# Optimization experiments

Hardware: AMD Instinct MI355X
Metric: run time of the kernel (lower is better)

## Reference

```python
import jax, jax.numpy as jnp
import numpy as np

B, S, D, H = 2, 1024, 1024, 16
HD = D // H
WINDOW = 256
FFN = 4 * D


def setup_inputs() -> dict:
    key = jax.random.key(0)
    ks = jax.random.split(key, 12)
    xav = lambda k, o, i: jax.random.normal(k, (o, i), jnp.float32) * np.sqrt(2.0 / (o + i))
    return {
        "x": jax.random.normal(ks[0], (B, S, D), jnp.float32),
        "wq": xav(ks[1], D, D), "bq": jnp.zeros((D,), jnp.float32),
        "wk": xav(ks[2], D, D), "bk": jnp.zeros((D,), jnp.float32),
        "wv": xav(ks[3], D, D), "bv": jnp.zeros((D,), jnp.float32),
        "wo": xav(ks[4], D, D), "bo": jnp.zeros((D,), jnp.float32),
        "attn_norm_w": jnp.ones((D,), jnp.float32),
        "ffn_norm_w": jnp.ones((D,), jnp.float32),
        "gate_w": xav(ks[5], FFN, D),
        "up_w": xav(ks[6], FFN, D),
        "down_w": xav(ks[7], D, FFN),
    }


def _rms(x, w):
    return x * jax.lax.rsqrt(jnp.mean(x * x, axis=-1, keepdims=True) + 1e-6) * w


def _rotate_half(x):
    x1, x2 = jnp.split(x, 2, axis=-1)
    return jnp.concatenate([-x2, x1], axis=-1)


def _rope_cos_sin(seq_len, head_dim):
    inv_freq = 1.0 / (10000.0 ** (jnp.arange(0, head_dim, 2, dtype=jnp.float32) / head_dim))
    freqs = jnp.arange(seq_len, dtype=jnp.float32)[:, None] * inv_freq[None, :]  # [S, HD/2]
    emb = jnp.concatenate([freqs, freqs], axis=-1)  # [S, HD]
    return jnp.cos(emb)[None, None], jnp.sin(emb)[None, None]  # [1,1,S,HD]


def reference(x, wq, bq, wk, bk, wv, bv, wo, bo, attn_norm_w, ffn_norm_w, gate_w, up_w, down_w):
    b, s, d = x.shape
    scale = 1.0 / np.sqrt(HD)
    residual = x
    h = _rms(x, attn_norm_w)
    q = (h @ wq.T + bq).reshape(b, s, H, HD).transpose(0, 2, 1, 3)  # [B,H,S,HD]
    k = (h @ wk.T + bk).reshape(b, s, H, HD).transpose(0, 2, 1, 3)
    v = (h @ wv.T + bv).reshape(b, s, H, HD).transpose(0, 2, 1, 3)
    cos, sin = _rope_cos_sin(s, HD)
    q = q * cos + _rotate_half(q) * sin
    k = k * cos + _rotate_half(k) * sin
    scores = jnp.einsum("bhqd,bhkd->bhqk", q, k) * scale  # dense [B,H,S,S]
    i = jnp.arange(s)[:, None]
    j = jnp.arange(s)[None, :]
    local_mask = (j <= i) & (i - j < WINDOW)  # causal sliding window
    scores = jnp.where(local_mask[None, None], scores, -jnp.inf)
    attn = jax.nn.softmax(scores, axis=-1)
    out = jnp.einsum("bhqk,bhkd->bhqd", attn, v)
    out = out.transpose(0, 2, 1, 3).reshape(b, s, d) @ wo.T + bo
    x = residual + out
    residual = x
    h = _rms(x, ffn_norm_w)
    ffn = (jax.nn.silu(h @ gate_w.T) * (h @ up_w.T)) @ down_w.T
    return (residual + ffn, attn)
```

## Files before the change

kernel.cpp:

```cpp
#include <hip/hip_runtime.h>

typedef unsigned short u16;
typedef unsigned int u32;
typedef __attribute__((ext_vector_type(8))) short short8;
typedef __attribute__((ext_vector_type(4))) float f32x4;

__device__ __forceinline__ float b2fu(u32 u) {
  union { u32 i; float f; } v; v.i = u << 16; return v.f;
}
__device__ __forceinline__ u16 f2bu(float f) {
  union { float f; u32 i; } v; v.f = f;
  u32 r = (v.i + 0x7fffu + ((v.i >> 16) & 1u)) >> 16;
  return (u16)r;
}
__device__ __forceinline__ void gl_lds16(const void* g, void* l) {
  __builtin_amdgcn_global_load_lds((const __attribute__((address_space(1))) void*)g,
                                   (__attribute__((address_space(3))) void*)l, 16, 0, 0);
}
__device__ __forceinline__ short8 ld_lds_b8(const u16* p) {
  uint2 a = *(const uint2*)p;
  uint2 b = *(const uint2*)(p + 4);
  union { u32 u[4]; short8 s; } v;
  v.u[0] = a.x; v.u[1] = a.y; v.u[2] = b.x; v.u[3] = b.y;
  return v.s;
}

__global__ __launch_bounds__(256) void cvt_weights(
    const float* __restrict__ wq, const float* __restrict__ wk,
    const float* __restrict__ wv, const float* __restrict__ wo,
    const float* __restrict__ wg, const float* __restrict__ wu,
    const float* __restrict__ wd, u16* __restrict__ dst,
    const float* __restrict__ bq, const float* __restrict__ bk,
    const float* __restrict__ bv, float* __restrict__ bqkv)
{
  if (blockIdx.x >= 16384) {
    const int s = blockIdx.x - 16384;
    const float* bsrc = (s == 0) ? bq : (s == 1) ? bk : bv;
    const int o = threadIdx.x * 4;
    *(float4*)(bqkv + s * 1024 + o) = *(const float4*)(bsrc + o);
    return;
  }
  size_t e = ((size_t)blockIdx.x * 256 + threadIdx.x) * 4;
  size_t seg = e >> 20;
  const float* src; size_t soff;
  if      (seg == 0) { src = wq; soff = e; }
  else if (seg == 1) { src = wk; soff = e - ((size_t)1 << 20); }
  else if (seg == 2) { src = wv; soff = e - ((size_t)2 << 20); }
  else if (seg == 3) { src = wo; soff = e - ((size_t)3 << 20); }
  else if (seg < 12) {
    size_t idx = e - ((size_t)4 << 20);
    int rc = (int)(idx >> 10);
    int col = (int)(idx & 1023);
    int bi = rc >> 5, j = rc & 31;
    if (j < 16) { src = wg; soff = (size_t)(bi * 16 + j) * 1024 + col; }
    else        { src = wu; soff = (size_t)(bi * 16 + j - 16) * 1024 + col; }
  }
  else { src = wd; soff = e - ((size_t)12 << 20); }
  float4 v = *(const float4*)(src + soff);
  *(ushort4*)(dst + e) = make_ushort4(f2bu(v.x), f2bu(v.y), f2bu(v.z), f2bu(v.w));
}

__global__ __launch_bounds__(256) void rmsnorm_kernel(
    const float* __restrict__ x, const float* __restrict__ w, u16* __restrict__ out)
{
  const int row = blockIdx.x;
  const int t = threadIdx.x;
  float4 v = ((const float4*)(x + (size_t)row * 1024))[t];
  float ss = v.x * v.x + v.y * v.y + v.z * v.z + v.w * v.w;
#pragma unroll
  for (int m = 32; m > 0; m >>= 1) ss += __shfl_xor(ss, m, 64);
  __shared__ float red[4];
  if ((t & 63) == 0) red[t >> 6] = ss;
  __syncthreads();
  float tot = red[0] + red[1] + red[2] + red[3];
  float r = rsqrtf(tot * (1.0f / 1024.0f) + 1e-6f);
  float4 wv = ((const float4*)w)[t];
  ushort4 o = make_ushort4(f2bu(v.x * r * wv.x), f2bu(v.y * r * wv.y),
                           f2bu(v.z * r * wv.z), f2bu(v.w * r * wv.w));
  ((ushort4*)(out + (size_t)row * 1024))[t] = o;
}

template<int TMB, int TNB, int EPI, bool HAS_BIAS, bool HAS_RES, bool SPLIT>
__global__ __launch_bounds__(256) void gemm_bt(
    const u16* __restrict__ A, const u16* __restrict__ B, float* __restrict__ C,
    const float* __restrict__ bias, const float* __restrict__ res,
    int M, int N, int K, int lda,
    u16* __restrict__ P0, u16* __restrict__ P1, u16* __restrict__ P2)
{
  constexpr int BK = 32;
  constexpr int WTM = TMB / 2, WTN = TNB / 2;
  constexpr int MT = WTM / 16, NT = WTN / 16;
  __shared__ u16 As[TMB * BK];
  __shared__ u16 Bs[TNB * BK];
  const int t = threadIdx.x;
  const int w = t >> 6, l = t & 63;
  const int wm = (w >> 1) * WTM, wn = (w & 1) * WTN;
  const int lr = l & 15, lq = l >> 4;
  const int tile_m = blockIdx.y * TMB, tile_n = blockIdx.x * TNB;
  const int kb = SPLIT ? blockIdx.z * K : 0;
  if (SPLIT) C += (size_t)blockIdx.z * M * N;

  f32x4 acc[MT][NT] = {};

  const int sr = t >> 2;
  const int scs = (((t & 3) ^ ((t >> 3) & 3)) * 8);
  const int rsw = (lq ^ ((lr >> 1) & 3)) * 8;
  const u16* Ab = A + (size_t)(tile_m + sr) * lda + kb + scs;
  const u16* Bb = B + (size_t)(tile_n + sr) * lda + kb + scs;

  for (int kk = 0; kk < K; kk += BK) {
#pragma unroll
    for (int i = 0; i < TMB / 64; ++i)
      gl_lds16(Ab + kk + (size_t)i * 64 * lda, &As[t * 8 + i * 2048]);
#pragma unroll
    for (int i = 0; i < TNB / 64; ++i)
      gl_lds16(Bb + kk + (size_t)i * 64 * lda, &Bs[t * 8 + i * 2048]);
    __syncthreads();
    short8 af[MT], bfr[NT];
#pragma unroll
    for (int mt = 0; mt < MT; ++mt)
      af[mt] = *(const short8*)&As[(wm + mt * 16 + lr) * BK + rsw];
#pragma unroll
    for (int nt = 0; nt < NT; ++nt)
      bfr[nt] = *(const short8*)&Bs[(wn + nt * 16 + lr) * BK + rsw];
#pragma unroll
    for (int mt = 0; mt < MT; ++mt)
#pragma unroll
      for (int nt = 0; nt < NT; ++nt)
        acc[mt][nt] = __builtin_amdgcn_mfma_f32_16x16x32_bf16(af[mt], bfr[nt], acc[mt][nt], 0, 0, 0);
    __syncthreads();
  }

  if (EPI == 0) {
#pragma unroll
    for (int nt = 0; nt < NT; ++nt) {
      const int col = tile_n + wn + nt * 16 + lr;
      const float bv = HAS_BIAS ? bias[col] : 0.0f;
#pragma unroll
      for (int mt = 0; mt < MT; ++mt) {
        const int row0 = tile_m + wm + mt * 16 + lq * 4;
#pragma unroll
        for (int r = 0; r < 4; ++r) {
          const size_t off = (size_t)(row0 + r) * N + col;
          float v = acc[mt][nt][r] + bv;
          if (HAS_RES) v += res[off];
          C[off] = v;
        }
      }
    }
  } else if (EPI == 1) {
    const int colbase = tile_n + wn;
    const int seg = colbase >> 10;
    const int h = (colbase >> 6) & 15;
    u16* dstb = (seg == 0) ? P0 : (seg == 1) ? P1 : P2;
    float bv[NT];
#pragma unroll
    for (int nt = 0; nt < NT; ++nt) bv[nt] = bias[colbase + nt * 16 + lr];
#pragma unroll
    for (int mt = 0; mt < MT; ++mt) {
      const int row0 = tile_m + wm + mt * 16 + lq * 4;
#pragma unroll
      for (int r = 0; r < 4; ++r) {
        const int row = row0 + r;
        const int s = row & 1023, b = row >> 10;
        u16* dst = dstb + (((size_t)(b * 16 + h) << 10) + s) * 64;
        if (seg < 2) {
#pragma unroll
          for (int np = 0; np < 2; ++np) {
            const int i = np * 16 + lr;
            const float th = (float)s * exp2f(-0.4152410118609203f * (float)i);
            float sn, cs; __sincosf(th, &sn, &cs);
            const float g0 = acc[mt][np][r] + bv[np];
            const float g2 = acc[mt][np + 2][r] + bv[np + 2];
            dst[i]      = f2bu(g0 * cs - g2 * sn);
            dst[i + 32] = f2bu(g2 * cs + g0 * sn);
          }
        } else {
#pragma unroll
          for (int nt = 0; nt < NT; ++nt)
            dst[nt * 16 + lr] = f2bu(acc[mt][nt][r] + bv[nt]);
        }
      }
    }
  } else {
#pragma unroll
    for (int nt = 0; nt < NT; nt += 2) {
      const int feat = (((tile_n + wn + nt * 16) >> 5) << 4) + lr;
#pragma unroll
      for (int mt = 0; mt < MT; ++mt) {
        const int row0 = tile_m + wm + mt * 16 + lq * 4;
#pragma unroll
        for (int r = 0; r < 4; ++r) {
          const float g = acc[mt][nt][r];
          const float u = acc[mt][nt + 1][r];
          const float a = g / (1.0f + __expf(-g)) * u;
          P0[(size_t)(row0 + r) * (N >> 1) + feat] = f2bu(a);
        }
      }
    }
  }
}

__global__ __launch_bounds__(256) void reduce4_kernel(
    const float* __restrict__ p, const float* __restrict__ res, float* __restrict__ out)
{
  const size_t i = ((size_t)blockIdx.x * 256 + threadIdx.x) * 4;
  float4 a = *(const float4*)(p + i);
  float4 b = *(const float4*)(p + i + 2097152);
  float4 c = *(const float4*)(p + i + 2 * 2097152);
  float4 d = *(const float4*)(p + i + 3 * 2097152);
  float4 r = *(const float4*)(res + i);
  float4 o;
  o.x = r.x + a.x + b.x + c.x + d.x;
  o.y = r.y + a.y + b.y + c.y + d.y;
  o.z = r.z + a.z + b.z + c.z + d.z;
  o.w = r.w + a.w + b.w + c.w + d.w;
  *(float4*)(out + i) = o;
}

#define KP 68
#define PP 292

__global__ __launch_bounds__(256) void attn_kernel(
    const u16* __restrict__ qb, const u16* __restrict__ kb, const u16* __restrict__ vb,
    float* __restrict__ probs, u16* __restrict__ ctx)
{
  __shared__ u16 Kbuf[288 * KP];
  __shared__ u16 Vbuf[288 * KP];
  __shared__ float smax[2][32];
  __shared__ float ssum[2][32];
  u16* Pbuf = Kbuf;

  const int blk = blockIdx.x;
  const int qt = blk & 31, bh = blk >> 5;
  const int b = bh >> 4, h = bh & 15;
  const int q0 = qt << 5;
  const int kstart = (q0 > 255) ? (q0 - 255) : 0;
  const int span = q0 + 32 - kstart;
  const int t = threadIdx.x;
  const int w = t >> 6, l = t & 63;
  const int lr = l & 15, lq = l >> 4;
  const int mw = w & 1, nh = w >> 1;
  const size_t bhS = (size_t)bh << 10;

  {
    const u16* kg = kb + ((bhS + (size_t)kstart) << 6);
    const u16* vg = vb + ((bhS + (size_t)kstart) << 6);
    for (int idx = t; idx < 288 * 8; idx += 256) {
      const int r = idx >> 3, c = (idx & 7) << 3;
      uint4 kv4 = make_uint4(0, 0, 0, 0), vv4 = make_uint4(0, 0, 0, 0);
      if (r < span) {
        kv4 = *(const uint4*)&kg[(r << 6) + c];
        vv4 = *(const uint4*)&vg[(r << 6) + c];
      }
      *(uint2*)&Kbuf[r * KP + c]     = make_uint2(kv4.x, kv4.y);
      *(uint2*)&Kbuf[r * KP + c + 4] = make_uint2(kv4.z, kv4.w);
      *(uint2*)&Vbuf[r * KP + c]     = make_uint2(vv4.x, vv4.y);
      *(uint2*)&Vbuf[r * KP + c + 4] = make_uint2(vv4.z, vv4.w);
    }
  }
  short8 qa0, qa1;
  {
    const u16* qrow = qb + ((bhS + (size_t)(q0 + mw * 16 + lr)) << 6) + lq * 8;
    qa0 = *(const short8*)qrow;
    qa1 = *(const short8*)(qrow + 32);
  }
  __syncthreads();

  f32x4 acc[9];
#pragma unroll
  for (int i = 0; i < 9; ++i) acc[i] = (f32x4){0.f, 0.f, 0.f, 0.f};
#pragma unroll
  for (int i = 0; i < 9; ++i) {
    const int nt = nh + 2 * i;
    const u16* kr = &Kbuf[(nt * 16 + lr) * KP + lq * 8];
    short8 kf0 = ld_lds_b8(kr);
    short8 kf1 = ld_lds_b8(kr + 32);
    acc[i] = __builtin_amdgcn_mfma_f32_16x16x32_bf16(qa0, kf0, acc[i], 0, 0, 0);
    acc[i] = __builtin_amdgcn_mfma_f32_16x16x32_bf16(qa1, kf1, acc[i], 0, 0, 0);
  }

  const int rbase = mw * 16 + lq * 4;
  float rmax[4] = {-1e30f, -1e30f, -1e30f, -1e30f};
#pragma unroll
  for (int i = 0; i < 9; ++i) {
    const int jg = kstart + (nh + 2 * i) * 16 + lr;
#pragma unroll
    for (int r = 0; r < 4; ++r) {
      const int q = q0 + rbase + r;
      const bool valid = (jg >= q - 255) && (jg <= q);
      const float v = valid ? acc[i][r] * 0.125f : -1e30f;
      acc[i][r] = v;
      rmax[r] = fmaxf(rmax[r], v);
    }
  }
#pragma unroll
  for (int r = 0; r < 4; ++r) {
    float m_ = rmax[r];
    m_ = fmaxf(m_, __shfl_xor(m_, 1, 64));
    m_ = fmaxf(m_, __shfl_xor(m_, 2, 64));
    m_ = fmaxf(m_, __shfl_xor(m_, 4, 64));
    m_ = fmaxf(m_, __shfl_xor(m_, 8, 64));
    rmax[r] = m_;
  }
  if (lr == 0) {
#pragma unroll
    for (int r = 0; r < 4; ++r) smax[nh][rbase + r] = rmax[r];
  }
  __syncthreads();
#pragma unroll
  for (int r = 0; r < 4; ++r)
    rmax[r] = fmaxf(smax[0][rbase + r], smax[1][rbase + r]);
  float rsum[4] = {0.f, 0.f, 0.f, 0.f};
#pragma unroll
  for (int i = 0; i < 9; ++i)
#pragma unroll
    for (int r = 0; r < 4; ++r) {
      const float p = exp2f((acc[i][r] - rmax[r]) * 1.44269504f);
      acc[i][r] = p;
      rsum[r] += p;
    }
#pragma unroll
  for (int r = 0; r < 4; ++r) {
    float s_ = rsum[r];
    s_ += __shfl_xor(s_, 1, 64);
    s_ += __shfl_xor(s_, 2, 64);
    s_ += __shfl_xor(s_, 4, 64);
    s_ += __shfl_xor(s_, 8, 64);
    rsum[r] = s_;
  }
  if (lr == 0) {
#pragma unroll
    for (int r = 0; r < 4; ++r) ssum[nh][rbase + r] = rsum[r];
  }
  __syncthreads();

  float inv4[4];
#pragma unroll
  for (int r = 0; r < 4; ++r)
    inv4[r] = 1.0f / (ssum[0][rbase + r] + ssum[1][rbase + r]);
#pragma unroll
  for (int i = 0; i < 9; ++i) {
    const int nt = nh + 2 * i;
#pragma unroll
    for (int r = 0; r < 4; ++r)
      Pbuf[(rbase + r) * PP + nt * 16 + lr] = f2bu(acc[i][r] * inv4[r]);
  }
  __syncthreads();

  {
    const int row = t >> 3;
    const int q = q0 + row;
    const int c0 = (t & 7) << 7;
    const int lo = q - 255;
    float* prow = probs + ((bhS + (size_t)q) << 10) + c0;
    const u16* pr = &Pbuf[row * PP];
#pragma unroll 4
    for (int cc = 0; cc < 128; cc += 4) {
      const int c = c0 + cc;
      float4 o;
      o.x = (c + 0 >= lo && c + 0 <= q) ? b2fu(pr[c + 0 - kstart]) : 0.0f;
      o.y = (c + 1 >= lo && c + 1 <= q) ? b2fu(pr[c + 1 - kstart]) : 0.0f;
      o.z = (c + 2 >= lo && c + 2 <= q) ? b2fu(pr[c + 2 - kstart]) : 0.0f;
      o.w = (c + 3 >= lo && c + 3 <= q) ? b2fu(pr[c + 3 - kstart]) : 0.0f;
      *(float4*)&prow[cc] = o;
    }
  }

  const int n0 = (w >> 1) * 2;
  f32x4 oacc[2] = {};
#pragma unroll
  for (int ks = 0; ks < 9; ++ks) {
    short8 pa = ld_lds_b8(&Pbuf[(mw * 16 + lr) * PP + ks * 32 + lq * 8]);
#pragma unroll
    for (int nn = 0; nn < 2; ++nn) {
      const int d = (n0 + nn) * 16 + lr;
      union { u16 u[8]; short8 s; } bf_;
#pragma unroll
      for (int jj = 0; jj < 8; ++jj)
        bf_.u[jj] = Vbuf[(ks * 32 + lq * 8 + jj) * KP + d];
      oacc[nn] = __builtin_amdgcn_mfma_f32_16x16x32_bf16(pa, bf_.s, oacc[nn], 0, 0, 0);
    }
  }
#pragma unroll
  for (int nn = 0; nn < 2; ++nn) {
    const int d = (n0 + nn) * 16 + lr;
#pragma unroll
    for (int r = 0; r < 4; ++r) {
      const int q = q0 + rbase + r;
      ctx[(((size_t)(b * 1024 + q)) << 10) + (h << 6) + d] = f2bu(oacc[nn][r]);
    }
  }
}

extern "C" void kernel_launch(void* const* d_in, const int* in_sizes, int n_in,
                              void* d_out, int out_size, void* d_ws, size_t ws_size,
                              hipStream_t stream) {
  (void)in_sizes; (void)n_in; (void)out_size; (void)ws_size;
  const float* x   = (const float*)d_in[0];
  const float* wq  = (const float*)d_in[1];
  const float* bq  = (const float*)d_in[2];
  const float* wk  = (const float*)d_in[3];
  const float* bk  = (const float*)d_in[4];
  const float* wv  = (const float*)d_in[5];
  const float* bv  = (const float*)d_in[6];
  const float* wo  = (const float*)d_in[7];
  const float* bo  = (const float*)d_in[8];
  const float* anw = (const float*)d_in[9];
  const float* fnw = (const float*)d_in[10];
  const float* wg  = (const float*)d_in[11];
  const float* wu  = (const float*)d_in[12];
  const float* wd  = (const float*)d_in[13];

  char* ws = (char*)d_ws;
  u16*   wbf  = (u16*)ws;
  float* bqkv = (float*)(ws + ((size_t)32 << 20));
  u16*   h1   = (u16*)(ws + ((size_t)32 << 20) + (16 << 10));
  char*  R    = ws + ((size_t)36 << 20) + (16 << 10);
  u16*   qbp  = (u16*)R;
  u16*   kbp  = (u16*)(R + ((size_t)4 << 20));
  u16*   vbp  = (u16*)(R + ((size_t)8 << 20));
  u16*   ctx  = (u16*)(R + ((size_t)12 << 20));
  float* x1   = (float*)(R + ((size_t)16 << 20));
  u16*   h2   = (u16*)(R + ((size_t)24 << 20));
  u16*   act  = (u16*)(R + ((size_t)28 << 20));
  float* pbuf = (float*)(R + ((size_t)44 << 20));

  float* out0  = (float*)d_out;
  float* probs = (float*)d_out + 2097152;

  cvt_weights<<<16387, 256, 0, stream>>>(wq, wk, wv, wo, wg, wu, wd, wbf,
                                          bq, bk, bv, bqkv);

  rmsnorm_kernel<<<2048, 256, 0, stream>>>(x, anw, h1);
  gemm_bt<128, 128, 1, true, false, false><<<dim3(24, 16), 256, 0, stream>>>(
      h1, wbf, nullptr, bqkv, nullptr, 2048, 3072, 1024, 1024, qbp, kbp, vbp);
  attn_kernel<<<1024, 256, 0, stream>>>(qbp, kbp, vbp, probs, ctx);
  gemm_bt<64, 128, 0, true, true, false><<<dim3(8, 32), 256, 0, stream>>>(
      ctx, wbf + ((size_t)3 << 20), x1, bo, x, 2048, 1024, 1024, 1024,
      nullptr, nullptr, nullptr);

  rmsnorm_kernel<<<2048, 256, 0, stream>>>(x1, fnw, h2);
  gemm_bt<128, 128, 2, false, false, false><<<dim3(64, 16), 256, 0, stream>>>(
      h2, wbf + ((size_t)4 << 20), nullptr, nullptr, nullptr, 2048, 8192, 1024, 1024,
      act, nullptr, nullptr);
  gemm_bt<128, 128, 0, false, false, true><<<dim3(8, 16, 4), 256, 0, stream>>>(
      act, wbf + ((size_t)12 << 20), pbuf, nullptr, nullptr, 2048, 1024, 1024, 4096,
      nullptr, nullptr, nullptr);
  reduce4_kernel<<<2048, 256, 0, stream>>>(pbuf, x1, out0);
}
```

Before: 424.7 us.

## Add 256x256-tile 8-wave ping-pong GEMM kernel for fused gate/up FFN

Replaces the generic 128x128 gemm_bt for the gate/up projection with a dedicated 512-thread kernel using 256x256 tiles, double-buffered LDS via direct global-to-LDS loads, XOR-swizzled LDS reads, and a four-phase schedule that interleaves staging, barriers and MFMA bursts with setprio. It aims to raise arithmetic intensity and hide load latency for the largest GEMM. It uses 128KB of LDS per block and a large accumulator footprint, which may limit occupancy to one block per CU despite launch_bounds(512,2). The grid (32x8=256 blocks) roughly matches the CU count.

New measurement: 410.5 us. 3.4% less time.

```diff
diff --git a/kernel.cpp b/kernel.cpp
--- a/kernel.cpp
+++ b/kernel.cpp
@@ -201,6 +201,102 @@
   }
 }
 
+#define FPH(buf, kk, mth, dostage, dovm) do {                                                  \
+    if ((mth) == 0) {                                                                          \
+      _Pragma("unroll")                                                                        \
+      for (int nt = 0; nt < 4; ++nt)                                                           \
+        bfr[nt] = *(const short8*)&Bs[(buf) * 16384 + (wn + nt * 16 + lr) * 64 +               \
+                                      (((kk) * 32 + lq * 8) ^ cxor)];                          \
+    }                                                                                          \
+    short8 af[4];                                                                              \
+    _Pragma("unroll")                                                                          \
+    for (int mt = 0; mt < 4; ++mt)                                                             \
+      af[mt] = *(const short8*)&As[(buf) * 16384 + (wm + (mth) * 64 + mt * 16 + lr) * 64 +     \
+                                   (((kk) * 32 + lq * 8) ^ cxor)];                             \
+    if (dostage) STAGE_ALL(kt + 1);                                                            \
+    __builtin_amdgcn_s_barrier();                                                              \
+    asm volatile("s_waitcnt lgkmcnt(0)" ::: "memory");                                         \
+    __builtin_amdgcn_sched_barrier(0);                                                         \
+    __builtin_amdgcn_s_setprio(1);                                                             \
+    _Pragma("unroll")                                                                          \
+    for (int mt = 0; mt < 4; ++mt)                                                             \
+      _Pragma("unroll")                                                                        \
+      for (int nt = 0; nt < 4; ++nt)                                                           \
+        acc[(mth) * 4 + mt][nt] =                                                              \
+            __builtin_amdgcn_mfma_f32_16x16x32_bf16(af[mt], bfr[nt], acc[(mth) * 4 + mt][nt],  \
+                                                    0, 0, 0);                                  \
+    __builtin_amdgcn_s_setprio(0);                                                             \
+    if (dovm) asm volatile("s_waitcnt vmcnt(0)" ::: "memory");                                 \
+    __builtin_amdgcn_s_barrier();                                                              \
+  } while (0)
+
+__global__ __launch_bounds__(512, 2) void ffn1_8ph(
+    const u16* __restrict__ A, const u16* __restrict__ B, u16* __restrict__ act)
+{
+  __shared__ u16 As[32768];
+  __shared__ u16 Bs[32768];
+  const int t = threadIdx.x;
+  const int wid = t >> 6, l = t & 63;
+  const int lr = l & 15, lq = l >> 4;
+  const int wm = (wid >> 2) * 128, wn = (wid & 3) * 64;
+  const int tile_m = blockIdx.y * 256, tile_n = blockIdx.x * 256;
+  const int cxor = (lr & 7) * 8;
+
+  const int srow = t >> 3;
+  const int schunk = (t & 7) ^ (srow & 7);
+  const u16* aRow = A + (size_t)(tile_m + srow) * 1024 + schunk * 8;
+  const u16* bRow = B + (size_t)(tile_n + srow) * 1024 + schunk * 8;
+
+  auto STAGE_ALL = [&](int kt2) {
+    if (kt2 < 16) {
+      const int bz2 = kt2 & 1;
+      const u16* ga = aRow + kt2 * 64;
+      const u16* gb = bRow + kt2 * 64;
+      u16* da = As + bz2 * 16384 + t * 8;
+      u16* db = Bs + bz2 * 16384 + t * 8;
+      gl_lds16(ga, da);
+      gl_lds16(ga + 64 * 1024, da + 4096);
+      gl_lds16(ga + 128 * 1024, da + 8192);
+      gl_lds16(ga + 192 * 1024, da + 12288);
+      gl_lds16(gb, db);
+      gl_lds16(gb + 64 * 1024, db + 4096);
+      gl_lds16(gb + 128 * 1024, db + 8192);
+      gl_lds16(gb + 192 * 1024, db + 12288);
+    }
+  };
+
+  f32x4 acc[8][4] = {};
+  short8 bfr[4];
+
+  STAGE_ALL(0);
+  asm volatile("s_waitcnt vmcnt(0)" ::: "memory");
+  __builtin_amdgcn_s_barrier();
+
+  for (int kt = 0; kt < 16; ++kt) {
+    const int bz = kt & 1;
+    FPH(bz, 0, 0, 1, 0);
+    FPH(bz, 0, 1, 0, 0);
+    FPH(bz, 1, 0, 0, 0);
+    FPH(bz, 1, 1, 0, 1);
+  }
+
+#pragma unroll
+  for (int nt = 0; nt < 4; nt += 2) {
+    const int feat = (((tile_n + wn + nt * 16) >> 5) << 4) + lr;
+#pragma unroll
+    for (int mi = 0; mi < 8; ++mi) {
+      const int row0 = tile_m + wm + mi * 16 + lq * 4;
+#pragma unroll
+      for (int r = 0; r < 4; ++r) {
+        const float g = acc[mi][nt][r];
+        const float u = acc[mi][nt + 1][r];
+        const float a = g / (1.0f + __expf(-g)) * u;
+        act[(size_t)(row0 + r) * 4096 + feat] = f2bu(a);
+      }
+    }
+  }
+}
+
 __global__ __launch_bounds__(256) void reduce4_kernel(
     const float* __restrict__ p, const float* __restrict__ res, float* __restrict__ out)
 {
@@ -441,9 +537,7 @@
       nullptr, nullptr, nullptr);
 
   rmsnorm_kernel<<<2048, 256, 0, stream>>>(x1, fnw, h2);
-  gemm_bt<128, 128, 2, false, false, false><<<dim3(64, 16), 256, 0, stream>>>(
-      h2, wbf + ((size_t)4 << 20), nullptr, nullptr, nullptr, 2048, 8192, 1024, 1024,
-      act, nullptr, nullptr);
+  ffn1_8ph<<<dim3(32, 8), 512, 0, stream>>>(h2, wbf + ((size_t)4 << 20), act);
   gemm_bt<128, 128, 0, false, false, true><<<dim3(8, 16, 4), 256, 0, stream>>>(
       act, wbf + ((size_t)12 << 20), pbuf, nullptr, nullptr, 2048, 1024, 1024, 4096,
       nullptr, nullptr, nullptr);
```
